# Kernel tuning notes

Hardware: AMD Instinct MI355X
Metric: run time of the kernel (lower is better)

The kernel has to match this reference:

```python
import jax, jax.numpy as jnp
import numpy as np

NEG = jnp.float32(-1e30)  # log-space 'zero' (avoids -inf NaNs)


def _ctc_loss(predictions, targets, pred_lengths, target_lengths, blank=0):
    # predictions: (B, T, C) log-probs; targets: (B, L) int labels (no blanks)
    B, T, C = predictions.shape
    L = targets.shape[1]
    S = 2 * L + 1  # extended label sequence: blank-interleaved

    ext = jnp.full((B, S), blank, dtype=targets.dtype).at[:, 1::2].set(targets)  # (B, S)
    # emission log-prob of each lattice state at each time step: (B, T, S)
    emit = jnp.take_along_axis(
        predictions, jnp.broadcast_to(ext[:, None, :], (B, T, S)), axis=2)

    # skip transition (s-2 -> s) allowed iff ext[s] != blank and ext[s] != ext[s-2]
    ext_m2 = jnp.pad(ext, ((0, 0), (2, 0)), constant_values=-1)[:, :S]
    skip = (ext != blank) & (ext != ext_m2)  # (B, S)

    alpha0 = jnp.full((B, S), NEG, dtype=predictions.dtype)
    alpha0 = alpha0.at[:, 0].set(emit[:, 0, 0]).at[:, 1].set(emit[:, 0, 1])

    emit_t = jnp.swapaxes(emit, 0, 1)  # (T, B, S)
    pad1 = jnp.full((B, 1), NEG, dtype=predictions.dtype)
    pad2 = jnp.full((B, 2), NEG, dtype=predictions.dtype)

    def step(alpha, xs):
        e_t, t = xs
        a1 = alpha
        a2 = jnp.concatenate([pad1, alpha[:, :-1]], axis=1)
        a3 = jnp.where(skip, jnp.concatenate([pad2, alpha[:, :-2]], axis=1), NEG)
        new = jax.nn.logsumexp(jnp.stack([a1, a2, a3], axis=0), axis=0) + e_t
        # freeze lattice beyond each example's input length
        new = jnp.where((t < pred_lengths)[:, None], new, alpha)
        return new, None

    alpha_T, _ = jax.lax.scan(step, alpha0, (emit_t[1:], jnp.arange(1, T)))

    tl = target_lengths.astype(jnp.int32)
    l1 = jnp.take_along_axis(alpha_T, (2 * tl - 1)[:, None], axis=1)[:, 0]
    l2 = jnp.take_along_axis(alpha_T, (2 * tl)[:, None], axis=1)[:, 0]
    per_ex = -jnp.logaddexp(l1, l2)
    # zero_infinity=True
    per_ex = jnp.where(per_ex > jnp.float32(1e29), 0.0, per_ex)
    # reduction='mean': divide by target length, then batch mean
    return jnp.mean(per_ex / jnp.maximum(tl, 1).astype(per_ex.dtype))


def setup_inputs() -> dict:
    key = jax.random.key(0)
    k1, k2, k3 = jax.random.split(key, 3)
    B, T, C, L = 128, 1024, 128, 128
    predictions = jax.random.normal(k1, (B, T, C), dtype=jnp.float32)
    targets = jax.random.randint(k2, (B, L), 1, C, dtype=jnp.int32)  # no blank (=0)
    pred_lengths = jnp.full((B,), T, dtype=jnp.int32)
    target_lengths = jax.random.randint(k3, (B,), L // 2, L + 1, dtype=jnp.int32)
    return {"predictions": predictions, "targets": targets,
            "pred_lengths": pred_lengths, "target_lengths": target_lengths}


def reference(predictions, targets, pred_lengths, target_lengths):
    return _ctc_loss(predictions, targets, pred_lengths, target_lengths, blank=0)
```

## Files before the change

kernel.cpp:

```cpp
#include <hip/hip_runtime.h>


static constexpr float LOG2E_F = 1.4426950408889634f;
static constexpr float LN2_F   = 0.6931471805599453f;

#if __has_builtin(__builtin_amdgcn_exp2f)
#define FEXP2(x) __builtin_amdgcn_exp2f(x)
#else
#define FEXP2(x) exp2f(x)
#endif
#if __has_builtin(__builtin_amdgcn_logf)
#define FLOG2(x) __builtin_amdgcn_logf(x)
#else
#define FLOG2(x) log2f(x)
#endif

typedef __attribute__((address_space(3))) uint32_t lds_u32_t;
typedef const __attribute__((address_space(1))) uint32_t glb_u32_t;

__device__ __forceinline__ float dpp_shr1(float src, float fill) {
  return __int_as_float(__builtin_amdgcn_update_dpp(
      __float_as_int(fill), __float_as_int(src), 0x138, 0xF, 0xF, false));
}
__device__ __forceinline__ int dpp_shr1_i(int src, int fill) {
  return __builtin_amdgcn_update_dpp(fill, src, 0x138, 0xF, 0xF, false);
}

template <int T, int C, int L>
__global__ __launch_bounds__(64) void ctc_alpha_lin2(
    const float* __restrict__ pred,
    const int*   __restrict__ targets,
    const int*   __restrict__ pred_len,
    const int*   __restrict__ tgt_len,
    float*       __restrict__ per_ex)
{
  constexpr int ROWS    = 64;
  constexpr int CHUNK_F = ROWS * C;
  constexpr int NCH     = T / ROWS;
  constexpr int S       = 2 * L + 1;

  __shared__ float emis[3 * CHUNK_F];
  __shared__ float afin[S];

  const int b = blockIdx.x;
  const int l = threadIdx.x;

  const float* __restrict__ prow = pred + (size_t)b * T * C;
  const int plen = pred_len[b];
  int tl = tgt_len[b]; if (tl < 1) tl = 1; if (tl > L) tl = L;

  const int cc1 = targets[b * L + 2 * l];
  const int cc3 = targets[b * L + 2 * l + 1];
  const float k1 = (l == 0) ? 0.0f
                  : ((cc1 != targets[b * L + 2 * l - 1]) ? 1.0f : 0.0f);
  const float k3 = (cc3 != cc1) ? 1.0f : 0.0f;

  auto stage = [&](int c) {
    const float* src0 = prow + (size_t)c * CHUNK_F + (l << 2);
    float* dst0 = &emis[(c % 3) * CHUNK_F];
#pragma unroll
    for (int i = 0; i < 32; ++i) {
      __builtin_amdgcn_global_load_lds((glb_u32_t*)(src0 + (i << 8)),
                                       (lds_u32_t*)(dst0 + (i << 8)),
                                       16, 0, 0);
    }
  };

  stage(0); stage(1);
  asm volatile("s_waitcnt vmcnt(32)" ::: "memory");

  float a0 = FEXP2(emis[0] * LOG2E_F);
  float x1 = (l == 0) ? FEXP2(emis[cc1] * LOG2E_F) : 0.0f;
  float x2 = 0.0f, x3 = 0.0f, x4 = 0.0f;
  int   E  = 0;

  const int tmax = plen < T ? plen : T;

  auto step = [&](float Eb, float E1, float E3) {
    const int Eprev = dpp_shr1_i(E, E);
    const uint32_t orx = __float_as_uint(x1) | __float_as_uint(x2) |
                         __float_as_uint(x3) | __float_as_uint(x4);
    if (orx == 0u) E = Eprev;
    int dE = Eprev - E;
    dE = dE < -126 ? -126 : (dE > 126 ? 126 : dE);
    const float sc = __int_as_float((dE + 127) << 23);
    const float P4 = dpp_shr1(x4, a0) * sc;
    const float P3 = dpp_shr1(x3, x3) * sc;
    const float t1 = fmaf(k1, P3, x1 + P4);
    const float t2 = x2 + x1;
    const float t3 = fmaf(k3, x1, x3 + x2);
    const float t4 = x4 + x3;
    x1 = t1 * E1; x2 = t2 * Eb; x3 = t3 * E3; x4 = t4 * Eb;
    a0 *= Eb;
  };

  auto renorm = [&]() {
    const float m = fmaxf(fmaxf(fmaxf(x1, x2), fmaxf(x3, x4)), a0);
    int ebi = (int)((__float_as_uint(m) >> 23) & 0xffu);
    if (ebi == 0) ebi = 126;
    const float sc = __uint_as_float((uint32_t)(253 - ebi) << 23);
    x1 *= sc; x2 *= sc; x3 *= sc; x4 *= sc; a0 *= sc;
    E += ebi - 126;
  };

  auto loadg = [&](float (&gb)[8], float (&g1)[8], float (&g3)[8], int r0) {
#pragma unroll
    for (int j = 0; j < 8; ++j) {
      int rr = r0 + j; if (rr > T - 1) rr = T - 1;
      const int rb = ((rr >> 6) % 3) * CHUNK_F + (rr & 63) * C;
      gb[j] = FEXP2(emis[rb]       * LOG2E_F);
      g1[j] = FEXP2(emis[rb + cc1] * LOG2E_F);
      g3[j] = FEXP2(emis[rb + cc3] * LOG2E_F);
    }
  };

#pragma unroll
  for (int t = 1; t < 16; ++t) {
    if (t == 8) renorm();
    if (t < tmax) {
      const int rb = t * C;
      step(FEXP2(emis[rb]       * LOG2E_F),
           FEXP2(emis[rb + cc1] * LOG2E_F),
           FEXP2(emis[rb + cc3] * LOG2E_F));
    }
  }

  float Ab[8], A1[8], A3[8], Bb[8], B1[8], B3[8];
  loadg(Ab, A1, A3, 16);

  for (int t0 = 16; t0 + 16 <= T; t0 += 16) {
    if ((t0 & 63) == 16) {
      const int c = t0 >> 6;
      if (c + 2 < NCH) {
        stage(c + 2);
        asm volatile("s_waitcnt vmcnt(32)" ::: "memory");
      } else {
        asm volatile("s_waitcnt vmcnt(0)" ::: "memory");
      }
    }
    loadg(Bb, B1, B3, t0 + 8);
    renorm();
    if (t0 + 16 <= tmax) {
#pragma unroll
      for (int j = 0; j < 8; ++j) step(Ab[j], A1[j], A3[j]);
      loadg(Ab, A1, A3, t0 + 16);
      renorm();
#pragma unroll
      for (int j = 0; j < 8; ++j) step(Bb[j], B1[j], B3[j]);
    } else {
#pragma unroll
      for (int j = 0; j < 8; ++j)
        if (t0 + j < tmax) step(Ab[j], A1[j], A3[j]);
      loadg(Ab, A1, A3, t0 + 16);
      renorm();
#pragma unroll
      for (int j = 0; j < 8; ++j)
        if (t0 + 8 + j < tmax) step(Bb[j], B1[j], B3[j]);
    }
  }

  const float fE = (float)E;
  afin[4 * l + 1] = FLOG2(x1) + fE;
  afin[4 * l + 2] = FLOG2(x2) + fE;
  afin[4 * l + 3] = FLOG2(x3) + fE;
  afin[4 * l + 4] = FLOG2(x4) + fE;
  if (l == 0) afin[0] = FLOG2(a0) + fE;
  __syncthreads();
  if (l == 0) {
    const float l1 = afin[2 * tl - 1];
    const float l2 = afin[2 * tl];
    const float mm = fmaxf(l1, l2);
    const float ls = mm + FLOG2(FEXP2(l1 - mm) + FEXP2(l2 - mm));
    float per = -(ls * LN2_F);
    if (!(per < 1e29f)) per = 0.0f;
    per_ex[b] = per / (float)tl;
  }
}

__global__ void ctc_reduce_kernel(const float* __restrict__ per_ex,
                                  float* __restrict__ out, int B)
{
  const int l = threadIdx.x;
  float v = 0.0f;
  for (int i = l; i < B; i += 64) v += per_ex[i];
#pragma unroll
  for (int off = 32; off > 0; off >>= 1) v += __shfl_down(v, off);
  if (l == 0) out[0] = v / (float)B;
}

extern "C" void kernel_launch(void* const* d_in, const int* in_sizes, int n_in,
                              void* d_out, int out_size, void* d_ws, size_t ws_size,
                              hipStream_t stream)
{
  const float* pred    = (const float*)d_in[0];
  const int*   targets = (const int*)d_in[1];
  const int*   plen    = (const int*)d_in[2];
  const int*   tlen    = (const int*)d_in[3];
  float*       out     = (float*)d_out;
  float*       ws      = (float*)d_ws;

  constexpr int B = 128, T = 1024, C = 128, L = 128;

  hipLaunchKernelGGL((ctc_alpha_lin2<T, C, L>), dim3(B), dim3(64), 0, stream,
                     pred, targets, plen, tlen, ws);
  hipLaunchKernelGGL(ctc_reduce_kernel, dim3(1), dim3(64), 0, stream,
                     ws, out, B);
}
```

Before: 193.7 us.

## Add producer warps that build exp'd emission tables for recurrence warp

Restructures the kernel into warp specialization: three producer waves gather the needed emission columns from global memory, exponentiate them, and write compact double-buffered LDS tables. One consumer wave runs the alpha recurrence from those tables. The full-row async global-to-LDS staging and the per-step exp on the critical path are gone. The final reduction kernel is replaced by a memset plus an atomicAdd, at the cost of a per-chunk block barrier and scattered global loads.

```diff
diff --git a/kernel.cpp b/kernel.cpp
--- a/kernel.cpp
+++ b/kernel.cpp
@@ -15,9 +15,6 @@
 #define FLOG2(x) log2f(x)
 #endif
 
-typedef __attribute__((address_space(3))) uint32_t lds_u32_t;
-typedef const __attribute__((address_space(1))) uint32_t glb_u32_t;
-
 __device__ __forceinline__ float dpp_shr1(float src, float fill) {
   return __int_as_float(__builtin_amdgcn_update_dpp(
       __float_as_int(fill), __float_as_int(src), 0x138, 0xF, 0xF, false));
@@ -27,54 +24,66 @@
 }
 
 template <int T, int C, int L>
-__global__ __launch_bounds__(64) void ctc_alpha_lin2(
+__global__ __launch_bounds__(256) void ctc_alpha_tab(
     const float* __restrict__ pred,
     const int*   __restrict__ targets,
     const int*   __restrict__ pred_len,
     const int*   __restrict__ tgt_len,
-    float*       __restrict__ per_ex)
+    float*       __restrict__ out,
+    float inv_B)
 {
-  constexpr int ROWS    = 64;
-  constexpr int CHUNK_F = ROWS * C;
-  constexpr int NCH     = T / ROWS;
-  constexpr int S       = 2 * L + 1;
+  constexpr int S   = 2 * L + 1;
+  constexpr int NCH = T / 64;
 
-  __shared__ float emis[3 * CHUNK_F];
-  __shared__ float afin[S];
+  __shared__ float2 tb13[2][64][64];
+  __shared__ float  tbB [2][64];
+  __shared__ float  afin[S];
 
-  const int b = blockIdx.x;
-  const int l = threadIdx.x;
+  const int b   = blockIdx.x;
+  const int tid = threadIdx.x;
+  const int wid = tid >> 6;
+  const int l   = tid & 63;
 
   const float* __restrict__ prow = pred + (size_t)b * T * C;
   const int plen = pred_len[b];
   int tl = tgt_len[b]; if (tl < 1) tl = 1; if (tl > L) tl = L;
+  const int tmax = plen < T ? plen : T;
 
-  const int cc1 = targets[b * L + 2 * l];
-  const int cc3 = targets[b * L + 2 * l + 1];
-  const float k1 = (l == 0) ? 0.0f
-                  : ((cc1 != targets[b * L + 2 * l - 1]) ? 1.0f : 0.0f);
-  const float k3 = (cc3 != cc1) ? 1.0f : 0.0f;
+  int bj = 0, btr = 0, bc1 = 0, bc3 = 0;
+  if (wid) {
+    const int gl = (wid - 1) * 64 + l;
+    bj  = gl & 63;
+    btr = gl >> 6;
+    bc1 = targets[b * L + 2 * bj];
+    bc3 = targets[b * L + 2 * bj + 1];
+  }
 
-  auto stage = [&](int c) {
-    const float* src0 = prow + (size_t)c * CHUNK_F + (l << 2);
-    float* dst0 = &emis[(c % 3) * CHUNK_F];
+  auto build = [&](int c) {
+    const int buf = c & 1;
+    const float* base = prow + (size_t)c * 64 * C;
 #pragma unroll
-    for (int i = 0; i < 32; ++i) {
-      __builtin_amdgcn_global_load_lds((glb_u32_t*)(src0 + (i << 8)),
-                                       (lds_u32_t*)(dst0 + (i << 8)),
-                                       16, 0, 0);
+    for (int i = 0; i < 22; ++i) {
+      const int t = btr + 3 * i;
+      if (t < 64) {
+        const float v1 = base[t * C + bc1];
+        const float v3 = base[t * C + bc3];
+        tb13[buf][t][bj] = make_float2(FEXP2(v1 * LOG2E_F),
+                                       FEXP2(v3 * LOG2E_F));
+      }
     }
+    if (wid == 1) tbB[buf][l] = FEXP2(base[l * C] * LOG2E_F);
   };
 
-  stage(0); stage(1);
-  asm volatile("s_waitcnt vmcnt(32)" ::: "memory");
+  float k1 = 0.0f, k3 = 0.0f;
+  if (!wid) {
+    const int c1 = targets[b * L + 2 * l];
+    const int c3 = targets[b * L + 2 * l + 1];
+    k1 = (l == 0) ? 0.0f : ((c1 != targets[b * L + 2 * l - 1]) ? 1.0f : 0.0f);
+    k3 = (c3 != c1) ? 1.0f : 0.0f;
+  }
 
-  float a0 = FEXP2(emis[0] * LOG2E_F);
-  float x1 = (l == 0) ? FEXP2(emis[cc1] * LOG2E_F) : 0.0f;
-  float x2 = 0.0f, x3 = 0.0f, x4 = 0.0f;
+  float a0 = 0.0f, x1 = 0.0f, x2 = 0.0f, x3 = 0.0f, x4 = 0.0f;
   int   E  = 0;
-
-  const int tmax = plen < T ? plen : T;
 
   auto step = [&](float Eb, float E1, float E3) {
     const int Eprev = dpp_shr1_i(E, E);
@@ -103,89 +112,53 @@
     E += ebi - 126;
   };
 
-  auto loadg = [&](float (&gb)[8], float (&g1)[8], float (&g3)[8], int r0) {
-#pragma unroll
-    for (int j = 0; j < 8; ++j) {
-      int rr = r0 + j; if (rr > T - 1) rr = T - 1;
-      const int rb = ((rr >> 6) % 3) * CHUNK_F + (rr & 63) * C;
-      gb[j] = FEXP2(emis[rb]       * LOG2E_F);
-      g1[j] = FEXP2(emis[rb + cc1] * LOG2E_F);
-      g3[j] = FEXP2(emis[rb + cc3] * LOG2E_F);
+  if (wid) build(0);
+  __syncthreads();
+
+  for (int c = 0; c < NCH; ++c) {
+    if (wid) {
+      if (c + 1 < NCH) build(c + 1);
+    } else {
+      const int buf = c & 1;
+      int r = c * 64;
+      float2 fA = tb13[buf][0][l];  float bA = tbB[buf][0];
+      float2 fB = tb13[buf][1][l];  float bB = tbB[buf][1];
+      for (int p = 0; p < 32; ++p, r += 2) {
+        if (r && !(r & 7)) renorm();
+        if (r == 0) {
+          a0 = bA; x1 = (l == 0) ? fA.x : 0.0f;
+          x2 = x3 = x4 = 0.0f; E = 0;
+        } else if (r < tmax) {
+          step(bA, fA.x, fA.y);
+        }
+        if (p < 31) { const int lr = (r + 2) & 63;
+                      fA = tb13[buf][lr][l]; bA = tbB[buf][lr]; }
+        if (r + 1 < tmax) step(bB, fB.x, fB.y);
+        if (p < 31) { const int lr = (r + 3) & 63;
+                      fB = tb13[buf][lr][l]; bB = tbB[buf][lr]; }
+      }
     }
-  };
-
-#pragma unroll
-  for (int t = 1; t < 16; ++t) {
-    if (t == 8) renorm();
-    if (t < tmax) {
-      const int rb = t * C;
-      step(FEXP2(emis[rb]       * LOG2E_F),
-           FEXP2(emis[rb + cc1] * LOG2E_F),
-           FEXP2(emis[rb + cc3] * LOG2E_F));
-    }
+    __syncthreads();
   }
 
-  float Ab[8], A1[8], A3[8], Bb[8], B1[8], B3[8];
-  loadg(Ab, A1, A3, 16);
-
-  for (int t0 = 16; t0 + 16 <= T; t0 += 16) {
-    if ((t0 & 63) == 16) {
-      const int c = t0 >> 6;
-      if (c + 2 < NCH) {
-        stage(c + 2);
-        asm volatile("s_waitcnt vmcnt(32)" ::: "memory");
-      } else {
-        asm volatile("s_waitcnt vmcnt(0)" ::: "memory");
-      }
-    }
-    loadg(Bb, B1, B3, t0 + 8);
-    renorm();
-    if (t0 + 16 <= tmax) {
-#pragma unroll
-      for (int j = 0; j < 8; ++j) step(Ab[j], A1[j], A3[j]);
-      loadg(Ab, A1, A3, t0 + 16);
-      renorm();
-#pragma unroll
-      for (int j = 0; j < 8; ++j) step(Bb[j], B1[j], B3[j]);
-    } else {
-#pragma unroll
-      for (int j = 0; j < 8; ++j)
-        if (t0 + j < tmax) step(Ab[j], A1[j], A3[j]);
-      loadg(Ab, A1, A3, t0 + 16);
-      renorm();
-#pragma unroll
-      for (int j = 0; j < 8; ++j)
-        if (t0 + 8 + j < tmax) step(Bb[j], B1[j], B3[j]);
-    }
+  if (!wid) {
+    const float fE = (float)E;
+    afin[4 * l + 1] = FLOG2(x1) + fE;
+    afin[4 * l + 2] = FLOG2(x2) + fE;
+    afin[4 * l + 3] = FLOG2(x3) + fE;
+    afin[4 * l + 4] = FLOG2(x4) + fE;
+    if (l == 0) afin[0] = FLOG2(a0) + fE;
   }
-
-  const float fE = (float)E;
-  afin[4 * l + 1] = FLOG2(x1) + fE;
-  afin[4 * l + 2] = FLOG2(x2) + fE;
-  afin[4 * l + 3] = FLOG2(x3) + fE;
-  afin[4 * l + 4] = FLOG2(x4) + fE;
-  if (l == 0) afin[0] = FLOG2(a0) + fE;
   __syncthreads();
-  if (l == 0) {
+  if (tid == 0) {
     const float l1 = afin[2 * tl - 1];
     const float l2 = afin[2 * tl];
     const float mm = fmaxf(l1, l2);
     const float ls = mm + FLOG2(FEXP2(l1 - mm) + FEXP2(l2 - mm));
     float per = -(ls * LN2_F);
     if (!(per < 1e29f)) per = 0.0f;
-    per_ex[b] = per / (float)tl;
+    atomicAdd(out, (per / (float)tl) * inv_B);
   }
-}
-
-__global__ void ctc_reduce_kernel(const float* __restrict__ per_ex,
-                                  float* __restrict__ out, int B)
-{
-  const int l = threadIdx.x;
-  float v = 0.0f;
-  for (int i = l; i < B; i += 64) v += per_ex[i];
-#pragma unroll
-  for (int off = 32; off > 0; off >>= 1) v += __shfl_down(v, off);
-  if (l == 0) out[0] = v / (float)B;
 }
 
 extern "C" void kernel_launch(void* const* d_in, const int* in_sizes, int n_in,
@@ -197,12 +170,10 @@
   const int*   plen    = (const int*)d_in[2];
   const int*   tlen    = (const int*)d_in[3];
   float*       out     = (float*)d_out;
-  float*       ws      = (float*)d_ws;
 
   constexpr int B = 128, T = 1024, C = 128, L = 128;
 
-  hipLaunchKernelGGL((ctc_alpha_lin2<T, C, L>), dim3(B), dim3(64), 0, stream,
-                     pred, targets, plen, tlen, ws);
-  hipLaunchKernelGGL(ctc_reduce_kernel, dim3(1), dim3(64), 0, stream,
-                     ws, out, B);
+  hipMemsetAsync(out, 0, sizeof(float), stream);
+  hipLaunchKernelGGL((ctc_alpha_tab<T, C, L>), dim3(B), dim3(256), 0, stream,
+                     pred, targets, plen, tlen, out, 1.0f / (float)B);
 }
```

Result: slower. 201.7 us (+4.1%).
